# Kernel optimization log

Hardware: AMD Instinct MI355X
Metric: run time of the kernel (lower is better)

The kernel has to match this reference:

```python
import jax, jax.numpy as jnp
import numpy as np

N_NODES = 4096
N_EDGES = 131072  # avg degree 32
N_STEPS = 1000


def setup_inputs() -> dict:
    key = jax.random.key(0)
    k1, k2, k3 = jax.random.split(key, 3)
    # Transition matrices: positive entries so the evidence division is well-conditioned.
    Qt = jax.random.uniform(k1, (N_STEPS, 2, 2), minval=0.1, maxval=1.0, dtype=jnp.float32)
    edge_index_x_t = jax.random.randint(k2, (2, N_EDGES), 0, N_NODES)
    edge_index_x_start = jax.random.randint(k3, (2, N_EDGES), 0, N_NODES)
    return {
        "Qt": Qt,
        "edge_index_x_t": edge_index_x_t,
        "edge_index_x_start": edge_index_x_start,
        "t": 500,
        "num_nodes": N_NODES,
    }


def _edge_index_to_adj(edge_index, num_nodes):
    # Dense binary adjacency, matching torch edge_index_to_adj.
    adj = jnp.zeros((num_nodes, num_nodes), dtype=jnp.int32)
    return adj.at[edge_index[0], edge_index[1]].set(1)


def reference(Qt, edge_index_x_t, edge_index_x_start, t, num_nodes):
    # q(x_{t-1} | x_t, x_0) = (Q0[:, x_t] * Q_{t-1}[x_0, :]) / Q_t[x_0, x_t]
    Q_likelihood = Qt[0]        # (2, 2)
    Q_prior = Qt[t - 1]         # (2, 2)  (batch of 1 identical time)
    Q_evidence = Qt[t]          # (2, 2)

    adj_x_t = _edge_index_to_adj(edge_index_x_t, num_nodes)      # (N, N) in {0,1}
    adj_x_start = _edge_index_to_adj(edge_index_x_start, num_nodes)

    # likelihood[i,j,k] = Q_likelihood[k, adj_x_t[i,j]]
    likelihood = jnp.transpose(Q_likelihood[:, adj_x_t], (1, 2, 0))  # (N, N, 2)
    # prior[i,j,:] = Q_prior[adj_x_start[i,j], :]
    prior = Q_prior[adj_x_start]                                     # (N, N, 2)
    # evidence[i,j] = Q_evidence[adj_x_start[i,j], adj_x_t[i,j]]
    evidence = Q_evidence[adj_x_start, adj_x_t][..., None]           # (N, N, 1)

    q_backward = likelihood * prior / evidence                       # (N, N, 2)

    # block_diag of a single triu(N,N,diag=1) mask == upper triangle (all possible edges)
    iu, ju = jnp.triu_indices(num_nodes, k=1)
    # forward returns q_backward_all[:, 1]
    return q_backward[iu, ju, 1]                                     # (N*(N-1)/2,)
```

## Files before the change

kernel.cpp:

```cpp
#include <hip/hip_runtime.h>
#include <cstdint>

#define N_NODES 4096
#define N_EDGES 131072
#define OUT_ELEMS (N_NODES * (N_NODES - 1) / 2)
#define OUT_QUADS (OUT_ELEMS / 4)
#define BM_WORDS_PAD 262144

__device__ __forceinline__ void compute_vals(const float* __restrict__ Qt,
                                             const int* __restrict__ t_ptr,
                                             float* vals) {
    const int t = t_ptr[0];
    const float l0 = Qt[2], l1 = Qt[3];
    const float p0 = Qt[(t - 1) * 4 + 1], p1 = Qt[(t - 1) * 4 + 3];
    const float e00 = Qt[t * 4 + 0], e01 = Qt[t * 4 + 1];
    const float e10 = Qt[t * 4 + 2], e11 = Qt[t * 4 + 3];
    vals[0] = l0 * p0 / e00;
    vals[1] = l1 * p0 / e01;
    vals[2] = l0 * p1 / e10;
    vals[3] = l1 * p1 / e11;
}

__device__ __forceinline__ int tri_idx(int i, int j) {
    return i * (2 * N_NODES - i - 1) / 2 + (j - i - 1);
}

__global__ void gt_build_bitmaps(const int* __restrict__ et,
                                 const int* __restrict__ es,
                                 uint32_t* __restrict__ bm) {
    int e = blockIdx.x * blockDim.x + threadIdx.x;
    const int* __restrict__ lst;
    uint32_t* __restrict__ map;
    if (e < N_EDGES) {
        lst = et;
        map = bm;
    } else {
        lst = es;
        map = bm + BM_WORDS_PAD;
        e -= N_EDGES;
    }
    int i = lst[e];
    int j = lst[N_EDGES + e];
    if (i < j) {
        int k = tri_idx(i, j);
        atomicOr(&map[k >> 5], 1u << (k & 31));
    }
}

__global__ void gt_write(const float* __restrict__ Qt,
                         const int* __restrict__ t_ptr,
                         const uint32_t* __restrict__ bm,
                         float4* __restrict__ out) {
    float vals[4];
    compute_vals(Qt, t_ptr, vals);

    int tid = blockIdx.x * blockDim.x + threadIdx.x;
    int w = tid >> 3;
    int sh = (tid & 7) * 4;
    uint32_t wt = bm[w] >> sh;
    uint32_t ws = bm[BM_WORDS_PAD + w] >> sh;

    float r[4];
#pragma unroll
    for (int k = 0; k < 4; ++k) {
        bool bt = (wt >> k) & 1u;
        bool bs = (ws >> k) & 1u;
        r[k] = bs ? (bt ? vals[3] : vals[2]) : (bt ? vals[1] : vals[0]);
    }
    out[tid] = make_float4(r[0], r[1], r[2], r[3]);
}

extern "C" void kernel_launch(void* const* d_in, const int* in_sizes, int n_in,
                              void* d_out, int out_size, void* d_ws, size_t ws_size,
                              hipStream_t stream) {
    const float* Qt = (const float*)d_in[0];
    const int* et = (const int*)d_in[1];
    const int* es = (const int*)d_in[2];
    const int* t_ptr = (const int*)d_in[3];
    float* out = (float*)d_out;
    uint32_t* bm = (uint32_t*)d_ws;

    hipMemsetAsync(bm, 0, 2 * BM_WORDS_PAD * sizeof(uint32_t), stream);
    gt_build_bitmaps<<<(2 * N_EDGES) / 256, 256, 0, stream>>>(et, es, bm);
    gt_write<<<OUT_QUADS / 256, 256, 0, stream>>>(Qt, t_ptr, bm, (float4*)out);
}
```

Measured before the change: 83.70 us.

## Fuse memset, bitmap build and output write into one cooperative kernel

Replaces the memset and the two kernel launches with a single cooperative kernel of 1024 blocks. Grid-wide syncs separate three phases: zeroing the bitmaps, the atomic bitmap build, and a grid-stride output write. This removes two launch and inter-kernel gaps. In exchange it pays for two grid barriers and runs the write phase with fewer resident threads, each looping over many quads.

```diff
diff --git a/kernel.cpp b/kernel.cpp
--- a/kernel.cpp
+++ b/kernel.cpp
@@ -1,11 +1,17 @@
 #include <hip/hip_runtime.h>
+#include <hip/hip_cooperative_groups.h>
 #include <cstdint>
+
+namespace cg = cooperative_groups;
 
 #define N_NODES 4096
 #define N_EDGES 131072
 #define OUT_ELEMS (N_NODES * (N_NODES - 1) / 2)
 #define OUT_QUADS (OUT_ELEMS / 4)
 #define BM_WORDS_PAD 262144
+#define NBLK 1024
+#define NTHR 256
+#define NTOT (NBLK * NTHR)
 
 __device__ __forceinline__ void compute_vals(const float* __restrict__ Qt,
                                              const int* __restrict__ t_ptr,
@@ -25,49 +31,51 @@
     return i * (2 * N_NODES - i - 1) / 2 + (j - i - 1);
 }
 
-__global__ void gt_build_bitmaps(const int* __restrict__ et,
-                                 const int* __restrict__ es,
-                                 uint32_t* __restrict__ bm) {
-    int e = blockIdx.x * blockDim.x + threadIdx.x;
-    const int* __restrict__ lst;
-    uint32_t* __restrict__ map;
-    if (e < N_EDGES) {
-        lst = et;
-        map = bm;
-    } else {
-        lst = es;
-        map = bm + BM_WORDS_PAD;
-        e -= N_EDGES;
+__global__ void __launch_bounds__(NTHR)
+gt_fused(const float* __restrict__ Qt,
+         const int* __restrict__ t_ptr,
+         const int* __restrict__ et,
+         const int* __restrict__ es,
+         uint32_t* __restrict__ bm,
+         float4* __restrict__ out) {
+    cg::grid_group grid = cg::this_grid();
+    const int tid = blockIdx.x * blockDim.x + threadIdx.x;
+
+    reinterpret_cast<uint2*>(bm)[tid] = make_uint2(0u, 0u);
+
+    grid.sync();
+
+    {
+        const bool is_t = (tid < N_EDGES);
+        const int* __restrict__ lst = is_t ? et : es;
+        uint32_t* __restrict__ map = is_t ? bm : bm + BM_WORDS_PAD;
+        const int e = is_t ? tid : tid - N_EDGES;
+        const int i = lst[e];
+        const int j = lst[N_EDGES + e];
+        if (i < j) {
+            const int k = tri_idx(i, j);
+            atomicOr(&map[k >> 5], 1u << (k & 31));
+        }
     }
-    int i = lst[e];
-    int j = lst[N_EDGES + e];
-    if (i < j) {
-        int k = tri_idx(i, j);
-        atomicOr(&map[k >> 5], 1u << (k & 31));
-    }
-}
 
-__global__ void gt_write(const float* __restrict__ Qt,
-                         const int* __restrict__ t_ptr,
-                         const uint32_t* __restrict__ bm,
-                         float4* __restrict__ out) {
+    grid.sync();
+
     float vals[4];
     compute_vals(Qt, t_ptr, vals);
-
-    int tid = blockIdx.x * blockDim.x + threadIdx.x;
-    int w = tid >> 3;
-    int sh = (tid & 7) * 4;
-    uint32_t wt = bm[w] >> sh;
-    uint32_t ws = bm[BM_WORDS_PAD + w] >> sh;
-
-    float r[4];
+    for (int q = tid; q < OUT_QUADS; q += NTOT) {
+        const int w = q >> 3;
+        const int sh = (q & 7) * 4;
+        const uint32_t wt = bm[w] >> sh;
+        const uint32_t ws = bm[BM_WORDS_PAD + w] >> sh;
+        float r[4];
 #pragma unroll
-    for (int k = 0; k < 4; ++k) {
-        bool bt = (wt >> k) & 1u;
-        bool bs = (ws >> k) & 1u;
-        r[k] = bs ? (bt ? vals[3] : vals[2]) : (bt ? vals[1] : vals[0]);
+        for (int k = 0; k < 4; ++k) {
+            const bool bt = (wt >> k) & 1u;
+            const bool bs = (ws >> k) & 1u;
+            r[k] = bs ? (bt ? vals[3] : vals[2]) : (bt ? vals[1] : vals[0]);
+        }
+        out[q] = make_float4(r[0], r[1], r[2], r[3]);
     }
-    out[tid] = make_float4(r[0], r[1], r[2], r[3]);
 }
 
 extern "C" void kernel_launch(void* const* d_in, const int* in_sizes, int n_in,
@@ -77,10 +85,11 @@
     const int* et = (const int*)d_in[1];
     const int* es = (const int*)d_in[2];
     const int* t_ptr = (const int*)d_in[3];
-    float* out = (float*)d_out;
+    float4* out = (float4*)d_out;
     uint32_t* bm = (uint32_t*)d_ws;
 
-    hipMemsetAsync(bm, 0, 2 * BM_WORDS_PAD * sizeof(uint32_t), stream);
-    gt_build_bitmaps<<<(2 * N_EDGES) / 256, 256, 0, stream>>>(et, es, bm);
-    gt_write<<<OUT_QUADS / 256, 256, 0, stream>>>(Qt, t_ptr, bm, (float4*)out);
+    void* args[] = {(void*)&Qt, (void*)&t_ptr, (void*)&et, (void*)&es,
+                    (void*)&bm, (void*)&out};
+    hipLaunchCooperativeKernel((void*)gt_fused, dim3(NBLK), dim3(NTHR), args, 0,
+                               stream);
 }
```

Result: slower. 248.7 us (+197.1%).
